# Kernel tuning notes

Hardware: AMD Instinct MI355X
Metric: run time of the kernel (lower is better)

The kernel has to match this reference:

```python
import jax, jax.numpy as jnp
import numpy as np

N = 32768          # total nodes
B = 64             # number of graphs (batch.max()+1)
IN_C = 256
OUT_C = 256
NUM_SCALES = 4
NUM_HEADS = 8
BN_EPS = 1e-5


def setup_inputs() -> dict:
    key = jax.random.key(0)
    ks = jax.random.split(key, 10)
    out_s = OUT_C // NUM_SCALES
    x = jax.random.normal(ks[0], (N, IN_C), jnp.float32)
    spectral = jax.random.normal(ks[1], (NUM_SCALES, N, IN_C), jnp.float32)
    batch = jnp.sort(jax.random.randint(ks[2], (N,), 0, B)).astype(jnp.int64)
    # per-scale Linear weights (glorot) and zero biases; stored as [S, in, out_s]
    g = (6.0 / (IN_C + out_s)) ** 0.5
    Ws = jax.random.uniform(ks[3], (NUM_SCALES, IN_C, out_s), jnp.float32, -g, g)
    bs = jnp.zeros((NUM_SCALES, out_s), jnp.float32)
    # MultiheadAttention params (torch layout: in_proj [3E,E], out_proj [E,E])
    s_in = (1.0 / OUT_C) ** 0.5
    W_in = jax.random.uniform(ks[4], (3 * OUT_C, OUT_C), jnp.float32, -s_in, s_in)
    b_in = jnp.zeros((3 * OUT_C,), jnp.float32)
    W_out = jax.random.uniform(ks[5], (OUT_C, OUT_C), jnp.float32, -s_in, s_in)
    b_out = jnp.zeros((OUT_C,), jnp.float32)
    gamma = jnp.ones((OUT_C,), jnp.float32)
    beta = jnp.zeros((OUT_C,), jnp.float32)
    return {"x": x, "spectral": spectral, "Ws": Ws, "bs": bs,
            "W_in": W_in, "b_in": b_in, "W_out": W_out, "b_out": b_out,
            "gamma": gamma, "beta": beta, "batch": batch}


def _forward(x, spectral, Ws, bs, W_in, b_in, W_out, b_out, gamma, beta, batch):
    n, E = x.shape[0], W_out.shape[0]
    # per-scale linear on (x + spectral_feat), concat over scales -> [N, E]
    scale_out = jnp.einsum('sni,sio->sno', x[None] + spectral, Ws) + bs[:, None, :]
    h = jnp.moveaxis(scale_out, 0, 1).reshape(n, E)
    # ragged -> dense padding (batch is sorted segment ids)
    counts = jnp.bincount(batch, length=B)
    max_nodes = int(np.asarray(counts).max())  # data-dependent pad, as in torch
    starts = jnp.concatenate([jnp.zeros((1,), counts.dtype), jnp.cumsum(counts)[:-1]])
    pos = jnp.arange(n) - starts[batch]
    h_pad = jnp.zeros((B, max_nodes, E), h.dtype).at[batch, pos].set(h)
    # MHA over padded graphs (no key-padding mask, matching the source)
    hd = E // NUM_HEADS
    qkv = h_pad @ W_in.T + b_in                       # [B, M, 3E]
    q, k, v = jnp.split(qkv, 3, axis=-1)
    def heads(t):
        return t.reshape(B, max_nodes, NUM_HEADS, hd).transpose(0, 2, 1, 3)
    q, k, v = heads(q) * (hd ** -0.5), heads(k), heads(v)
    attn = jax.nn.softmax(jnp.einsum('bhqd,bhkd->bhqk', q, k), axis=-1)
    ctx = jnp.einsum('bhqk,bhkd->bhqd', attn, v)
    ctx = ctx.transpose(0, 2, 1, 3).reshape(B, max_nodes, E)
    h_att = ctx @ W_out.T + b_out
    # dense -> ragged unpad
    h2 = h_att[batch, pos]                            # [N, E]
    # BatchNorm1d (training-mode batch stats, deterministic) + ReLU; dropout=eval
    mean = h2.mean(axis=0)
    var = h2.var(axis=0)
    hn = (h2 - mean) * jax.lax.rsqrt(var + BN_EPS) * gamma + beta
    return jax.nn.relu(hn)


def reference(x, spectral, Ws, bs, W_in, b_in, W_out, b_out, gamma, beta, batch):
    return _forward(x, spectral, Ws, bs, W_in, b_in, W_out, b_out, gamma, beta, batch)
```

## Files before the change

### kernel.cpp

```cpp
#include <hip/hip_runtime.h>


typedef __attribute__((ext_vector_type(8))) short frag8;
typedef __attribute__((ext_vector_type(4))) short frag4;
typedef __attribute__((ext_vector_type(4))) float f32x4;
typedef __attribute__((ext_vector_type(8))) unsigned short ushort8;
typedef __attribute__((ext_vector_type(2))) unsigned int uint2e;

#define NN 32768
#define NB 64
#define CIN 256
#define COUT 256
#define NHEAD 8
#define HD 32

#define BM 128
#define LDB 264
#define KT 128

#if __has_builtin(__builtin_amdgcn_mfma_f32_16x16x16bf16_1k)
#define HAS_MFMA16 1
#else
#define HAS_MFMA16 0
#endif

#if __has_builtin(__builtin_amdgcn_exp2f)
#define EXP2(x) __builtin_amdgcn_exp2f(x)
#else
#define EXP2(x) __expf((x) * 0.6931471805599453f)
#endif

#if __has_builtin(__builtin_amdgcn_global_load_lds)
#define HAS_GLDS 1
#else
#define HAS_GLDS 0
#endif

__device__ inline unsigned short f2bf(float f) {
  unsigned u = __builtin_bit_cast(unsigned, f);
  u += 0x7FFFu + ((u >> 16) & 1u);
  return (unsigned short)(u >> 16);
}
__device__ inline float bf2f(unsigned short h) {
  return __builtin_bit_cast(float, (unsigned)h << 16);
}
__device__ inline unsigned cvtpk(float a, float b) {
  unsigned r;
  asm("v_cvt_pk_bf16_f32 %0, %1, %2" : "=v"(r) : "v"(a), "v"(b));
  return r;
}

__device__ inline void gld16(const void* g, void* l) {
#if HAS_GLDS
  __builtin_amdgcn_global_load_lds(
      (const __attribute__((address_space(1))) unsigned int*)g,
      (__attribute__((address_space(3))) unsigned int*)l, 16, 0, 0);
#else
  int lane = threadIdx.x & 63;
  *(float4*)((char*)l + lane * 16) = *(const float4*)g;
#endif
}

__global__ void k_prep(const float* __restrict__ Ws, const float* __restrict__ Win,
                       const float* __restrict__ Wout, const int* __restrict__ batch,
                       unsigned short* __restrict__ wst, unsigned short* __restrict__ winb,
                       unsigned short* __restrict__ woutb, int* __restrict__ meta) {
  int tid = blockIdx.x * 256 + threadIdx.x;
  if (tid < NN) {
    int v = batch[tid];
    int prev = (tid == 0) ? -1 : batch[tid - 1];
    for (int bb = prev + 1; bb <= v; ++bb) meta[NB + bb] = tid;
  }
  if (tid < 4 * 64 * 256) {
    int s = tid >> 14, rem = tid & 16383, o = rem >> 8, i = rem & 255;
    wst[tid] = f2bf(Ws[((s * 256) + i) * 64 + o]);
  } else if (tid < 4 * 64 * 256 + 768 * 256) {
    int t2 = tid - 4 * 64 * 256;
    winb[t2] = f2bf(Win[t2]);
  } else if (tid < 4 * 64 * 256 + 768 * 256 + 256 * 256) {
    int t3 = tid - (4 * 64 * 256 + 768 * 256);
    woutb[t3] = f2bf(Wout[t3]);
  }
}
__global__ void k_meta2(int* __restrict__ meta) {
  __shared__ int mx[NB];
  int b = threadIdx.x;
  int s = meta[NB + b];
  int e = (b == 63) ? NN : meta[NB + b + 1];
  meta[b] = e - s;
  mx[b] = e - s;
  __syncthreads();
  if (b == 0) {
    int m = 0;
    for (int j = 0; j < NB; ++j) m = max(m, mx[j]);
    meta[2 * NB] = m;
  }
}

__device__ inline void stage_Bpanel(const unsigned short* __restrict__ Wt,
                                    unsigned short (*Bs)[LDB], int t) {
  int n = t >> 2, seg = t & 3;
  const unsigned short* src = Wt + (size_t)n * 256 + seg * 64;
#pragma unroll
  for (int i = 0; i < 8; ++i) {
    uint4 v = *(const uint4*)(src + i * 8);
    *(uint4*)&Bs[n][seg * 64 + i * 8] = v;
  }
}


__device__ inline void stage_chunk(const float* __restrict__ x,
                                   const float* __restrict__ sb,
                                   int r0, int kc, char* chunk, int t) {
  int w = t >> 6, lane = t & 63;
  const float* src = (w < 2) ? x : sb;
  char* base = chunk + (w >> 1) * 16384 + (w & 1) * 8192;
  int rlow = lane >> 3;
  int slot = lane & 7;
  int cswz = (slot ^ (rlow & 7)) << 2;
  const float* g0 = src + (size_t)(r0 + (w & 1) * 64 + rlow) * CIN + kc * 32 + cswz;
#pragma unroll
  for (int j = 0; j < 8; ++j)
    gld16(g0 + (size_t)j * 8 * CIN, base + j * 1024);
}

__global__ __launch_bounds__(256) void k_scale(const float* __restrict__ x,
                                               const float* __restrict__ spec,
                                               const unsigned short* __restrict__ wst,
                                               const float* __restrict__ bs,
                                               unsigned short* __restrict__ h) {
  __shared__ unsigned short Bs[64][LDB];
  __shared__ __align__(16) char chunk[32768];
  int t = threadIdx.x, lane = t & 63, wave = t >> 6;
  int r0 = blockIdx.x * BM, s = blockIdx.y;
  int m16 = lane & 15, quad = lane >> 4;

  const float* sbp = spec + (size_t)s * NN * CIN;

  stage_Bpanel(wst + (size_t)s * 64 * 256, Bs, t);
  stage_chunk(x, sbp, r0, 0, chunk, t);
  __syncthreads();

  f32x4 z = {0.f, 0.f, 0.f, 0.f};
  f32x4 acc[2][4];
#pragma unroll
  for (int mi = 0; mi < 2; ++mi)
#pragma unroll
    for (int ni = 0; ni < 4; ++ni) acc[mi][ni] = z;

  const char* xls = chunk;
  const char* sls = chunk + 16384;
  int sw = m16 & 7;
  int s0 = (((quad << 1)) ^ sw) << 4;
  int s1 = (((quad << 1) | 1) ^ sw) << 4;

#pragma unroll
  for (int kc = 0; kc < 8; ++kc) {
#pragma unroll
    for (int mi = 0; mi < 2; ++mi) {
      int rb = (wave * 32 + mi * 16 + m16) << 7;
      float4 xlo = *(const float4*)(xls + rb + s0);
      float4 xhi = *(const float4*)(xls + rb + s1);
      float4 plo = *(const float4*)(sls + rb + s0);
      float4 phi = *(const float4*)(sls + rb + s1);
      uint4 u;
      u.x = cvtpk(xlo.x + plo.x, xlo.y + plo.y);
      u.y = cvtpk(xlo.z + plo.z, xlo.w + plo.w);
      u.z = cvtpk(xhi.x + phi.x, xhi.y + phi.y);
      u.w = cvtpk(xhi.z + phi.z, xhi.w + phi.w);
      frag8 a = __builtin_bit_cast(frag8, u);
      frag8 b0 = *(const frag8*)&Bs[m16][kc * 32 + quad * 8];
      frag8 b1 = *(const frag8*)&Bs[16 + m16][kc * 32 + quad * 8];
      frag8 b2 = *(const frag8*)&Bs[32 + m16][kc * 32 + quad * 8];
      frag8 b3 = *(const frag8*)&Bs[48 + m16][kc * 32 + quad * 8];
      acc[mi][0] = __builtin_amdgcn_mfma_f32_16x16x32_bf16(a, b0, acc[mi][0], 0, 0, 0);
      acc[mi][1] = __builtin_amdgcn_mfma_f32_16x16x32_bf16(a, b1, acc[mi][1], 0, 0, 0);
      acc[mi][2] = __builtin_amdgcn_mfma_f32_16x16x32_bf16(a, b2, acc[mi][2], 0, 0, 0);
      acc[mi][3] = __builtin_amdgcn_mfma_f32_16x16x32_bf16(a, b3, acc[mi][3], 0, 0, 0);
    }
    __syncthreads();
    if (kc < 7) {
      stage_chunk(x, sbp, r0, kc + 1, chunk, t);
      __syncthreads();
    }
  }

#pragma unroll
  for (int mi = 0; mi < 2; ++mi)
#pragma unroll
    for (int ni = 0; ni < 4; ++ni) {
      int col = ni * 16 + m16;
      float bias = bs[s * 64 + col];
#pragma unroll
      for (int rp = 0; rp < 2; ++rp) {
        int row = r0 + wave * 32 + mi * 16 + quad * 4 + rp * 2;
        unsigned u = cvtpk(acc[mi][ni][rp * 2] + bias, acc[mi][ni][rp * 2 + 1] + bias);
        h[(size_t)row * COUT + s * 64 + col] = (unsigned short)u;
        h[(size_t)(row + 1) * COUT + s * 64 + col] = (unsigned short)(u >> 16);
      }
    }
}

template <int LDOUT, bool DOSTATS>
__global__ __launch_bounds__(256, 4) void k_lin(const unsigned short* __restrict__ A,
                                                const unsigned short* __restrict__ Wt,
                                                const float* __restrict__ bias,
                                                unsigned short* __restrict__ out,
                                                float* __restrict__ sums) {
  __shared__ unsigned short Bs[64][LDB];
  int t = threadIdx.x, lane = t & 63, wave = t >> 6;
  int r0 = blockIdx.x * BM, c0 = blockIdx.y * 64;
  int m16 = lane & 15, quad = lane >> 4;

  stage_Bpanel(Wt + (size_t)c0 * 256, Bs, t);

  const unsigned short* pa0 = A + (size_t)(r0 + wave * 32 + m16) * 256 + quad * 8;
  const unsigned short* pa1 = pa0 + 16 * 256;

  frag8 PA[3];
  PA[0] = *(const frag8*)(pa0);
  PA[1] = *(const frag8*)(pa1);
  PA[2] = *(const frag8*)(pa0 + 32);

  __syncthreads();

  f32x4 z = {0.f, 0.f, 0.f, 0.f};
  f32x4 acc[2][4];
#pragma unroll
  for (int mi = 0; mi < 2; ++mi)
#pragma unroll
    for (int ni = 0; ni < 4; ++ni) acc[mi][ni] = z;

#pragma unroll
  for (int st = 0; st < 16; ++st) {
    const int kc = st >> 1, mi = st & 1, slot = st % 3;
    frag8 a = PA[slot];
    if (st + 3 < 16) {
      const int nst = st + 3;
      PA[slot] = *(const frag8*)(((nst & 1) ? pa1 : pa0) + (nst >> 1) * 32);
    }
    frag8 b0 = *(const frag8*)&Bs[m16][kc * 32 + quad * 8];
    frag8 b1 = *(const frag8*)&Bs[16 + m16][kc * 32 + quad * 8];
    frag8 b2 = *(const frag8*)&Bs[32 + m16][kc * 32 + quad * 8];
    frag8 b3 = *(const frag8*)&Bs[48 + m16][kc * 32 + quad * 8];
    acc[mi][0] = __builtin_amdgcn_mfma_f32_16x16x32_bf16(a, b0, acc[mi][0], 0, 0, 0);
    acc[mi][1] = __builtin_amdgcn_mfma_f32_16x16x32_bf16(a, b1, acc[mi][1], 0, 0, 0);
    acc[mi][2] = __builtin_amdgcn_mfma_f32_16x16x32_bf16(a, b2, acc[mi][2], 0, 0, 0);
    acc[mi][3] = __builtin_amdgcn_mfma_f32_16x16x32_bf16(a, b3, acc[mi][3], 0, 0, 0);
  }

#pragma unroll
  for (int ni = 0; ni < 4; ++ni) {
    int col = c0 + ni * 16 + m16;
    float bv = bias[col];
    float s1 = 0.f, s2 = 0.f;
#pragma unroll
    for (int mi = 0; mi < 2; ++mi) {
#pragma unroll
      for (int rp = 0; rp < 2; ++rp) {
        float v0 = acc[mi][ni][rp * 2] + bv;
        float v1 = acc[mi][ni][rp * 2 + 1] + bv;
        if (DOSTATS) { s1 += v0 + v1; s2 += v0 * v0 + v1 * v1; }
        int row = r0 + wave * 32 + mi * 16 + quad * 4 + rp * 2;
        unsigned u = cvtpk(v0, v1);
        out[(size_t)row * LDOUT + col] = (unsigned short)u;
        out[(size_t)(row + 1) * LDOUT + col] = (unsigned short)(u >> 16);
      }
    }
    if (DOSTATS) {
      s1 += __shfl_xor(s1, 16); s1 += __shfl_xor(s1, 32);
      s2 += __shfl_xor(s2, 16); s2 += __shfl_xor(s2, 32);
      if (quad == 0) {
        atomicAdd(&sums[col], s1);
        atomicAdd(&sums[256 + col], s2);
      }
    }
  }
}

__global__ __launch_bounds__(256) void k_attn_mfma(const unsigned short* __restrict__ qkv,
                                                   const int* __restrict__ meta,
                                                   unsigned short* __restrict__ ctx) {
  int b = blockIdx.x >> 3, head = blockIdx.x & 7;
  int c = meta[b], st = meta[NB + b], M = meta[2 * NB];
  int q0 = blockIdx.y * 128;
  if (q0 >= c) return;

  __shared__ unsigned short Vt[32][KT + 8];

  int t = threadIdx.x, lane = t & 63, wave = t >> 6;
  int m16 = lane & 15, quad = lane >> 4;
  const float SC2 = 0.17677669529663687f * 1.4426950408889634f;
  float extra = (float)(M - c);

  int qbase = q0 + wave * 32;
  frag8 qf[2];
#pragma unroll
  for (int qg = 0; qg < 2; ++qg) {
    int qrow = qbase + qg * 16 + m16;
    qf[qg] = *(const frag8*)(qkv + (size_t)(st + qrow) * 768 + head * 32 + quad * 8);
  }

  f32x4 zz = {0.f, 0.f, 0.f, 0.f};
  f32x4 O[2][2];
  float lp[2] = {0.f, 0.f};
#pragma unroll
  for (int qg = 0; qg < 2; ++qg) { O[qg][0] = zz; O[qg][1] = zz; }

#if !HAS_MFMA16
  int sl0 = m16 + ((quad & 1) << 5);
  int sl1 = sl0 + 16;
#endif

  for (int kt = 0; kt < c; kt += KT) {
    {
      int key = t >> 1, dh0 = (t & 1) * 16;
      const unsigned short* vp = qkv + (size_t)(st + kt + key) * 768 + 512 + head * 32 + dh0;
      ushort8 v0 = *(const ushort8*)vp;
      ushort8 v1 = *(const ushort8*)(vp + 8);
#pragma unroll
      for (int i = 0; i < 8; ++i) {
        Vt[dh0 + i][key] = v0[i];
        Vt[dh0 + 8 + i][key] = v1[i];
      }
    }
    __syncthreads();

#pragma unroll
    for (int sub = 0; sub < 4; ++sub) {
      int ks = kt + sub * 32;
      if (ks < c) {
        bool full = (ks + 32 <= c);
        frag8 kf[2];
#pragma unroll
        for (int kh = 0; kh < 2; ++kh) {
          int krow = ks + kh * 16 + m16;
          kf[kh] = *(const frag8*)(qkv + (size_t)(st + krow) * 768 + 256 + head * 32 + quad * 8);
        }
        unsigned pk[2][2][2];
#pragma unroll
        for (int qg = 0; qg < 2; ++qg)
#pragma unroll
          for (int kh = 0; kh < 2; ++kh) {
            f32x4 s = __builtin_amdgcn_mfma_f32_16x16x32_bf16(kf[kh], qf[qg], zz, 0, 0, 0);
            float p[4];
#pragma unroll
            for (int r = 0; r < 4; ++r) p[r] = EXP2(s[r] * SC2);
            if (!full) {
#pragma unroll
              for (int r = 0; r < 4; ++r)
                if (ks + kh * 16 + quad * 4 + r >= c) p[r] = 0.f;
            }
            lp[qg] += (p[0] + p[1]) + (p[2] + p[3]);
            pk[qg][kh][0] = cvtpk(p[0], p[1]);
            pk[qg][kh][1] = cvtpk(p[2], p[3]);
          }
#if HAS_MFMA16
        frag4 vb[2][2];
#pragma unroll
        for (int kh = 0; kh < 2; ++kh)
#pragma unroll
          for (int dh = 0; dh < 2; ++dh)
            vb[kh][dh] = *(const frag4*)&Vt[dh * 16 + m16][sub * 32 + kh * 16 + quad * 4];
#pragma unroll
        for (int qg = 0; qg < 2; ++qg) {
          frag4 pa0 = __builtin_bit_cast(frag4, uint2e{pk[qg][0][0], pk[qg][0][1]});
          frag4 pa1 = __builtin_bit_cast(frag4, uint2e{pk[qg][1][0], pk[qg][1][1]});
#pragma unroll
          for (int dh = 0; dh < 2; ++dh) {
            O[qg][dh] = __builtin_amdgcn_mfma_f32_16x16x16bf16_1k(pa0, vb[0][dh], O[qg][dh], 0, 0, 0);
            O[qg][dh] = __builtin_amdgcn_mfma_f32_16x16x16bf16_1k(pa1, vb[1][dh], O[qg][dh], 0, 0, 0);
          }
        }
#else
        frag8 vf[2];
#pragma unroll
        for (int dh = 0; dh < 2; ++dh)
          vf[dh] = *(const frag8*)&Vt[dh * 16 + m16][sub * 32 + quad * 8];
#pragma unroll
        for (int qg = 0; qg < 2; ++qg) {
          unsigned a0 = __shfl(pk[qg][0][0], sl0), a1 = __shfl(pk[qg][0][1], sl0);
          unsigned a2 = __shfl(pk[qg][0][0], sl1), a3 = __shfl(pk[qg][0][1], sl1);
          unsigned b0 = __shfl(pk[qg][1][0], sl0), b1 = __shfl(pk[qg][1][1], sl0);
          unsigned b2 = __shfl(pk[qg][1][0], sl1), b3 = __shfl(pk[qg][1][1], sl1);
          uint4 pw;
          pw.x = (quad < 2) ? a0 : b0;
          pw.y = (quad < 2) ? a1 : b1;
          pw.z = (quad < 2) ? a2 : b2;
          pw.w = (quad < 2) ? a3 : b3;
          frag8 pf = __builtin_bit_cast(frag8, pw);
#pragma unroll
          for (int dh = 0; dh < 2; ++dh)
            O[qg][dh] = __builtin_amdgcn_mfma_f32_16x16x32_bf16(pf, vf[dh], O[qg][dh], 0, 0, 0);
        }
#endif
      }
    }
    __syncthreads();
  }

#pragma unroll
  for (int qg = 0; qg < 2; ++qg) {
    float v = lp[qg];
    v += __shfl_xor(v, 16);
    v += __shfl_xor(v, 32);
    lp[qg] = v;
  }

#pragma unroll
  for (int qg = 0; qg < 2; ++qg)
#pragma unroll
    for (int r = 0; r < 4; ++r) {
      int qrow = qbase + qg * 16 + quad * 4 + r;
      float lsum = __shfl(lp[qg], quad * 4 + r);
      if (qrow < c) {
        float inv = 1.f / (lsum + extra);
        unsigned short* op = ctx + (size_t)(st + qrow) * 256 + head * 32;
        unsigned u = cvtpk(O[qg][0][r] * inv, O[qg][1][r] * inv);
        op[m16] = (unsigned short)u;
        op[16 + m16] = (unsigned short)(u >> 16);
      }
    }
}

__global__ __launch_bounds__(256) void k_bn_apply(const unsigned short* __restrict__ h,
                                                  const float* __restrict__ sums,
                                                  const float* __restrict__ gamma,
                                                  const float* __restrict__ beta,
                                                  float* __restrict__ out) {
  size_t i8 = ((size_t)blockIdx.x * 256 + threadIdx.x) * 8;
  int c0 = (int)(i8 & 255);
  ushort8 v = *(const ushort8*)(h + i8);
  float4 o0, o1;
  float res[8];
#pragma unroll
  for (int i = 0; i < 8; ++i) {
    int ch = c0 + i;
    float mean = sums[ch] * (1.0f / NN);
    float var = sums[256 + ch] * (1.0f / NN) - mean * mean;
    float sc = rsqrtf(var + 1e-5f) * gamma[ch];
    float sh = beta[ch] - mean * sc;
    res[i] = fmaxf(bf2f(v[i]) * sc + sh, 0.f);
  }
  o0.x = res[0]; o0.y = res[1]; o0.z = res[2]; o0.w = res[3];
  o1.x = res[4]; o1.y = res[5]; o1.z = res[6]; o1.w = res[7];
  *(float4*)(out + i8) = o0;
  *(float4*)(out + i8 + 4) = o1;
}

extern "C" void kernel_launch(void* const* d_in, const int* in_sizes, int n_in,
                              void* d_out, int out_size, void* d_ws, size_t ws_size,
                              hipStream_t stream) {
  const float* x      = (const float*)d_in[0];
  const float* spec   = (const float*)d_in[1];
  const float* Ws     = (const float*)d_in[2];
  const float* bs     = (const float*)d_in[3];
  const float* Win    = (const float*)d_in[4];
  const float* b_in   = (const float*)d_in[5];
  const float* Wout   = (const float*)d_in[6];
  const float* b_out  = (const float*)d_in[7];
  const float* gamma  = (const float*)d_in[8];
  const float* beta   = (const float*)d_in[9];
  const int* batch    = (const int*)d_in[10];
  float* out = (float*)d_out;

  char* w = (char*)d_ws;
  size_t off = 0;
  auto alloc = [&](size_t bytes) -> void* {
    off = (off + 255) & ~(size_t)255;
    void* p = w + off; off += bytes; return p;
  };
  int* meta             = (int*)alloc(129 * sizeof(int));
  unsigned short* wst   = (unsigned short*)alloc((size_t)4 * 64 * 256 * 2);
  unsigned short* winb  = (unsigned short*)alloc((size_t)768 * 256 * 2);
  unsigned short* woutb = (unsigned short*)alloc((size_t)256 * 256 * 2);
  float* sums           = (float*)alloc(512 * 4);
  unsigned short* h     = (unsigned short*)alloc((size_t)NN * 256 * 2);
  unsigned short* qkv   = (unsigned short*)alloc((size_t)NN * 768 * 2);
  unsigned short* ctx   = (unsigned short*)alloc((size_t)NN * 256 * 2);
  unsigned short* hatt  = (unsigned short*)alloc((size_t)NN * 256 * 2);

  (void)hipMemsetAsync(sums, 0, 512 * 4, stream);
  k_prep<<<1280, 256, 0, stream>>>(Ws, Win, Wout, batch, wst, winb, woutb, meta);
  k_meta2<<<1, 64, 0, stream>>>(meta);
  k_scale<<<dim3(NN / BM, 4), 256, 0, stream>>>(x, spec, wst, bs, h);
  k_lin<768, false><<<dim3(NN / BM, 12), 256, 0, stream>>>(h, winb, b_in, qkv, nullptr);
  k_attn_mfma<<<dim3(NB * NHEAD, 8), 256, 0, stream>>>(qkv, meta, ctx);
  k_lin<256, true><<<dim3(NN / BM, 4), 256, 0, stream>>>(ctx, woutb, b_out, hatt, sums);
  k_bn_apply<<<NN * 256 / 2048, 256, 0, stream>>>(hatt, sums, gamma, beta, out);
}
```

Before: 419.0 us.

## Stage whole A tile as bf16 in LDS via register loads in k_scale

Replaces the per-k-chunk global_load_lds staging of fp32 x and spectral tiles with a single upfront pass. Each thread loads x and spectral rows into registers, adds and converts them to bf16, and stores the full 128x256 A tile in padded LDS. The MMA loop then runs without per-chunk barriers, reads the B fragments once per k-step, and no longer converts inside the loop. The cost is losing the overlap of global loads with compute, since all loads complete before any MFMA starts, and higher register pressure from holding many float4s.

```diff
diff --git a/kernel.cpp b/kernel.cpp
--- a/kernel.cpp
+++ b/kernel.cpp
@@ -16,6 +16,7 @@
 
 #define BM 128
 #define LDB 264
+#define LDA 264
 #define KT 128
 
 #if __has_builtin(__builtin_amdgcn_mfma_f32_16x16x16bf16_1k)
@@ -30,12 +31,6 @@
 #define EXP2(x) __expf((x) * 0.6931471805599453f)
 #endif
 
-#if __has_builtin(__builtin_amdgcn_global_load_lds)
-#define HAS_GLDS 1
-#else
-#define HAS_GLDS 0
-#endif
-
 __device__ inline unsigned short f2bf(float f) {
   unsigned u = __builtin_bit_cast(unsigned, f);
   u += 0x7FFFu + ((u >> 16) & 1u);
@@ -48,17 +43,6 @@
   unsigned r;
   asm("v_cvt_pk_bf16_f32 %0, %1, %2" : "=v"(r) : "v"(a), "v"(b));
   return r;
-}
-
-__device__ inline void gld16(const void* g, void* l) {
-#if HAS_GLDS
-  __builtin_amdgcn_global_load_lds(
-      (const __attribute__((address_space(1))) unsigned int*)g,
-      (__attribute__((address_space(3))) unsigned int*)l, 16, 0, 0);
-#else
-  int lane = threadIdx.x & 63;
-  *(float4*)((char*)l + lane * 16) = *(const float4*)g;
-#endif
 }
 
 __global__ void k_prep(const float* __restrict__ Ws, const float* __restrict__ Win,
@@ -109,36 +93,44 @@
 }
 
 
-__device__ inline void stage_chunk(const float* __restrict__ x,
-                                   const float* __restrict__ sb,
-                                   int r0, int kc, char* chunk, int t) {
-  int w = t >> 6, lane = t & 63;
-  const float* src = (w < 2) ? x : sb;
-  char* base = chunk + (w >> 1) * 16384 + (w & 1) * 8192;
-  int rlow = lane >> 3;
-  int slot = lane & 7;
-  int cswz = (slot ^ (rlow & 7)) << 2;
-  const float* g0 = src + (size_t)(r0 + (w & 1) * 64 + rlow) * CIN + kc * 32 + cswz;
-#pragma unroll
-  for (int j = 0; j < 8; ++j)
-    gld16(g0 + (size_t)j * 8 * CIN, base + j * 1024);
-}
-
 __global__ __launch_bounds__(256) void k_scale(const float* __restrict__ x,
                                                const float* __restrict__ spec,
                                                const unsigned short* __restrict__ wst,
                                                const float* __restrict__ bs,
                                                unsigned short* __restrict__ h) {
+  __shared__ unsigned short As[BM][LDA];
   __shared__ unsigned short Bs[64][LDB];
-  __shared__ __align__(16) char chunk[32768];
   int t = threadIdx.x, lane = t & 63, wave = t >> 6;
   int r0 = blockIdx.x * BM, s = blockIdx.y;
   int m16 = lane & 15, quad = lane >> 4;
 
+  stage_Bpanel(wst + (size_t)s * 64 * 256, Bs, t);
+
   const float* sbp = spec + (size_t)s * NN * CIN;
-
-  stage_Bpanel(wst + (size_t)s * 64 * 256, Bs, t);
-  stage_chunk(x, sbp, r0, 0, chunk, t);
+  int rA = wave * 32 + (lane >> 5);
+  int cA = (lane & 31) * 8;
+  const float* px = x + (size_t)(r0 + rA) * CIN + cA;
+  const float* ps = sbp + (size_t)(r0 + rA) * CIN + cA;
+#pragma unroll
+  for (int g = 0; g < 4; ++g) {
+    float4 xa[4][2], sa[4][2];
+#pragma unroll
+    for (int i = 0; i < 4; ++i) {
+      const float* px_ = px + (size_t)(g * 8 + i * 2) * CIN;
+      const float* ps_ = ps + (size_t)(g * 8 + i * 2) * CIN;
+      xa[i][0] = *(const float4*)px_;  xa[i][1] = *(const float4*)(px_ + 4);
+      sa[i][0] = *(const float4*)ps_;  sa[i][1] = *(const float4*)(ps_ + 4);
+    }
+#pragma unroll
+    for (int i = 0; i < 4; ++i) {
+      uint4 u;
+      u.x = cvtpk(xa[i][0].x + sa[i][0].x, xa[i][0].y + sa[i][0].y);
+      u.y = cvtpk(xa[i][0].z + sa[i][0].z, xa[i][0].w + sa[i][0].w);
+      u.z = cvtpk(xa[i][1].x + sa[i][1].x, xa[i][1].y + sa[i][1].y);
+      u.w = cvtpk(xa[i][1].z + sa[i][1].z, xa[i][1].w + sa[i][1].w);
+      *(uint4*)&As[rA + g * 8 + i * 2][cA] = u;
+    }
+  }
   __syncthreads();
 
   f32x4 z = {0.f, 0.f, 0.f, 0.f};
@@ -148,40 +140,19 @@
 #pragma unroll
     for (int ni = 0; ni < 4; ++ni) acc[mi][ni] = z;
 
-  const char* xls = chunk;
-  const char* sls = chunk + 16384;
-  int sw = m16 & 7;
-  int s0 = (((quad << 1)) ^ sw) << 4;
-  int s1 = (((quad << 1) | 1) ^ sw) << 4;
-
 #pragma unroll
   for (int kc = 0; kc < 8; ++kc) {
+    frag8 b0 = *(const frag8*)&Bs[m16][kc * 32 + quad * 8];
+    frag8 b1 = *(const frag8*)&Bs[16 + m16][kc * 32 + quad * 8];
+    frag8 b2 = *(const frag8*)&Bs[32 + m16][kc * 32 + quad * 8];
+    frag8 b3 = *(const frag8*)&Bs[48 + m16][kc * 32 + quad * 8];
 #pragma unroll
     for (int mi = 0; mi < 2; ++mi) {
-      int rb = (wave * 32 + mi * 16 + m16) << 7;
-      float4 xlo = *(const float4*)(xls + rb + s0);
-      float4 xhi = *(const float4*)(xls + rb + s1);
-      float4 plo = *(const float4*)(sls + rb + s0);
-      float4 phi = *(const float4*)(sls + rb + s1);
-      uint4 u;
-      u.x = cvtpk(xlo.x + plo.x, xlo.y + plo.y);
-      u.y = cvtpk(xlo.z + plo.z, xlo.w + plo.w);
-      u.z = cvtpk(xhi.x + phi.x, xhi.y + phi.y);
-      u.w = cvtpk(xhi.z + phi.z, xhi.w + phi.w);
-      frag8 a = __builtin_bit_cast(frag8, u);
-      frag8 b0 = *(const frag8*)&Bs[m16][kc * 32 + quad * 8];
-      frag8 b1 = *(const frag8*)&Bs[16 + m16][kc * 32 + quad * 8];
-      frag8 b2 = *(const frag8*)&Bs[32 + m16][kc * 32 + quad * 8];
-      frag8 b3 = *(const frag8*)&Bs[48 + m16][kc * 32 + quad * 8];
+      frag8 a = *(const frag8*)&As[wave * 32 + mi * 16 + m16][kc * 32 + quad * 8];
       acc[mi][0] = __builtin_amdgcn_mfma_f32_16x16x32_bf16(a, b0, acc[mi][0], 0, 0, 0);
       acc[mi][1] = __builtin_amdgcn_mfma_f32_16x16x32_bf16(a, b1, acc[mi][1], 0, 0, 0);
       acc[mi][2] = __builtin_amdgcn_mfma_f32_16x16x32_bf16(a, b2, acc[mi][2], 0, 0, 0);
       acc[mi][3] = __builtin_amdgcn_mfma_f32_16x16x32_bf16(a, b3, acc[mi][3], 0, 0, 0);
-    }
-    __syncthreads();
-    if (kc < 7) {
-      stage_chunk(x, sbp, r0, kc + 1, chunk, t);
-      __syncthreads();
     }
   }
 
```

After: 419.3 us. Within noise of the previous version (+0.1%).
